# Kernel optimization log

Hardware: AMD Instinct MI355X
Metric: run time of the kernel (lower is better)

Reference implementation:

```python
import jax, jax.numpy as jnp
import numpy as np

N = 100000   # nodes
E = 640000   # edges
IN = 256     # raw input feature dim
D = 128      # post-MLP node feature dim (fixed in FilterGNN)


def setup_inputs() -> dict:
    key = jax.random.key(0)
    ks = jax.random.split(key, 10)
    x = jax.random.normal(ks[0], (N, IN), jnp.float32)
    alpha = jax.random.uniform(ks[1], (E, 1), jnp.float32)  # edge gate logits in [0,1)
    edge_index = jax.random.randint(ks[2], (2, E), 0, N, dtype=jnp.int32)
    norm = jnp.ones((E,), jnp.float32)  # passed to message in the original but unused
    # MLP `lin`: in_channels -> 512 -> 256 -> 128 (kaiming-normal weights, zero bias)
    def kaiming(k, fan_out, fan_in):
        return jax.random.normal(k, (fan_out, fan_in), jnp.float32) * jnp.sqrt(2.0 / fan_in)
    W1 = kaiming(ks[3], 512, IN); b1 = jnp.zeros((512,), jnp.float32)
    W2 = kaiming(ks[4], 256, 512); b2 = jnp.zeros((256,), jnp.float32)
    W3 = kaiming(ks[5], D, 256);  b3 = jnp.zeros((D,), jnp.float32)
    return {"x": x, "alpha": alpha, "edge_index": edge_index, "norm": norm,
            "W1": W1, "b1": b1, "W2": W2, "b2": b2, "W3": W3, "b3": b3}


def reference(x, alpha, edge_index, norm, W1, b1, W2, b2, W3, b3):
    # FilterGNN.lin: Linear-Tanh-Linear-Tanh-Linear  -> [N, 128]
    h = jnp.tanh(x @ W1.T + b1)
    h = jnp.tanh(h @ W2.T + b2)
    h = h @ W3.T + b3
    # FilterGraphConv1: gather x_j, elementwise relu gate, scatter-mean over targets.
    # (The [-1, H, C] view with H*C = 128 is a pure reshape; the gate broadcasts
    #  over all features, so the math is identical without the head split.)
    src, dst = edge_index[0], edge_index[1]
    gate = 2.0 * jax.nn.relu(jax.lax.stop_gradient(alpha) - 0.5)  # [E, 1]
    msg = h[src] * gate                                           # [E, 128] gather + gate
    sums = jax.ops.segment_sum(msg, dst, num_segments=N)          # [N, 128]
    cnt = jax.ops.segment_sum(jnp.ones((E,), h.dtype), dst, num_segments=N)
    out = sums / jnp.maximum(cnt, 1.0)[:, None]                   # scatter-mean (0 if no edges)
    return out
```

## Files before the change

### kernel.cpp

```cpp
#include <hip/hip_runtime.h>

typedef __attribute__((ext_vector_type(8))) short short8;
typedef __attribute__((ext_vector_type(4))) float f32x4;

__device__ __forceinline__ unsigned short f2bf(float f) {
    union { float f; unsigned u; } v; v.f = f;
    unsigned r = v.u + 0x7FFFu + ((v.u >> 16) & 1u);
    return (unsigned short)(r >> 16);
}
__device__ __forceinline__ float bf2f(unsigned short h) {
    union { unsigned u; float f; } v; v.u = ((unsigned)h) << 16;
    return v.f;
}

__device__ __forceinline__ float tanh_fast(float x) {
    float xc = fminf(fmaxf(x, -9.0f), 9.0f);
    float t  = __expf(2.0f * xc);
    return (t - 1.0f) * __builtin_amdgcn_rcpf(t + 1.0f);
}

__device__ __forceinline__ unsigned long long pack4(float4 v) {
    return (unsigned long long)f2bf(v.x)
         | ((unsigned long long)f2bf(v.y) << 16)
         | ((unsigned long long)f2bf(v.z) << 32)
         | ((unsigned long long)f2bf(v.w) << 48);
}

#define GLD16(gptr, lptr)                                                     \
    __builtin_amdgcn_global_load_lds(                                         \
        (const __attribute__((address_space(1))) unsigned int*)(gptr),        \
        (__attribute__((address_space(3))) unsigned int*)(lptr), 16, 0, 0)

__global__ __launch_bounds__(256) void cast_w(
    const float* __restrict__ W1, unsigned short* __restrict__ w1bf,
    const float* __restrict__ W2, unsigned short* __restrict__ w2bf,
    const float* __restrict__ W3, unsigned short* __restrict__ w3bf)
{
    int t = blockIdx.x * 256 + threadIdx.x;
    const float* s; unsigned short* d; int q;
    if (t < 32768)      { s = W1; d = w1bf; q = t; }
    else if (t < 65536) { s = W2; d = w2bf; q = t - 32768; }
    else if (t < 73728) { s = W3; d = w3bf; q = t - 65536; }
    else return;
    int base = q * 4;
    float4 v = *(const float4*)(s + base);
    *(unsigned long long*)(d + base) = pack4(v);
}

__global__ __launch_bounds__(256) void gemm1(
    const float* __restrict__ x, const unsigned short* __restrict__ W1,
    const float* __restrict__ b1, unsigned short* __restrict__ C, int M)
{
    __shared__ __align__(16) short xs[128 * 256];
    __shared__ __align__(16) short Bs[128 * 64];

    const int tid  = threadIdx.x;
    const int wave = tid >> 6;
    const int lane = tid & 63;
    const int m0 = blockIdx.x * 128;
    const int wm = (wave >> 1) * 64;
    const int wn = (wave & 1) * 64;
    const int lm = lane & 15;
    const int quad = lane >> 4;
    const int srow = lane >> 3;
    const int scol = ((lane & 7) ^ srow) * 8;

    #pragma unroll 4
    for (int j = 0; j < 16; ++j) {
        int idx = j * 256 + tid;
        int r = idx >> 5, c = idx & 31;
        int gr = m0 + r; if (gr >= M) gr = M - 1;
        const float* p = x + (size_t)gr * 256 + c * 8;
        float4 a0 = *(const float4*)(p);
        float4 a1 = *(const float4*)(p + 4);
        unsigned long long* d = (unsigned long long*)
            &xs[r * 256 + (c >> 3) * 64 + (((c & 7) ^ (r & 7)) * 8)];
        d[0] = pack4(a0); d[1] = pack4(a1);
    }

    for (int nh = 0; nh < 4; ++nh) {
        const int n0 = nh * 128;
        f32x4 acc[4][4] = {};
        for (int kt = 0; kt < 4; ++kt) {
            const int k0 = kt * 64;
            #pragma unroll
            for (int i = 0; i < 4; ++i) {
                int r0 = wave * 32 + i * 8;
                GLD16(W1 + (size_t)(n0 + r0 + srow) * 256 + k0 + scol, &Bs[r0 * 64]);
            }
            __syncthreads();
            #pragma unroll
            for (int ks = 0; ks < 2; ++ks) {
                short8 af[4], bf_[4];
                const int cc = (((ks * 4 + quad) ^ (lm & 7)) * 8);
                #pragma unroll
                for (int i = 0; i < 4; ++i) {
                    af[i]  = *(const short8*)&xs[(wm + i * 16 + lm) * 256 + k0 + cc];
                    bf_[i] = *(const short8*)&Bs[(wn + i * 16 + lm) * 64 + cc];
                }
                #pragma unroll
                for (int im = 0; im < 4; ++im)
                    #pragma unroll
                    for (int in = 0; in < 4; ++in)
                        acc[im][in] = __builtin_amdgcn_mfma_f32_16x16x32_bf16(
                            af[im], bf_[in], acc[im][in], 0, 0, 0);
            }
            __syncthreads();
        }
        #pragma unroll
        for (int in = 0; in < 4; ++in) {
            int gn = n0 + wn + in * 16 + lm;
            float bb = b1[gn];
            #pragma unroll
            for (int im = 0; im < 4; ++im) {
                #pragma unroll
                for (int r = 0; r < 4; ++r) {
                    int gm = m0 + wm + im * 16 + quad * 4 + r;
                    if (gm < M)
                        C[(size_t)gm * 512 + gn] = f2bf(tanh_fast(acc[im][in][r] + bb));
                }
            }
        }
    }
}

__global__ __launch_bounds__(256) void gemm23(
    const unsigned short* __restrict__ h1, const unsigned short* __restrict__ W2,
    const float* __restrict__ b2, const unsigned short* __restrict__ W3,
    const float* __restrict__ b3, unsigned short* __restrict__ hout, int M)
{
    __shared__ __align__(16) short As[64][64];
    __shared__ __align__(16) short Bs[256][64];
    __shared__ __align__(16) short h2s[64][264];

    const int tid  = threadIdx.x;
    const int wave = tid >> 6;
    const int lane = tid & 63;
    const int m0 = blockIdx.x * 64;
    const int wm = (wave >> 1) * 32;
    const int lm = lane & 15;
    const int quad = lane >> 4;
    const int srow = lane >> 3;
    const int scol = ((lane & 7) ^ srow) * 8;
    const int cc0 = (quad ^ (lm & 7)) * 8;
    const int cc1 = ((4 + quad) ^ (lm & 7)) * 8;

    {
        const int wn = (wave & 1) * 128;
        f32x4 acc[2][8] = {};
        for (int k0 = 0; k0 < 512; k0 += 64) {
            #pragma unroll
            for (int i = 0; i < 2; ++i) {
                int r0 = wave * 16 + i * 8;
                int gr = m0 + r0 + srow; if (gr >= M) gr = M - 1;
                GLD16(h1 + (size_t)gr * 512 + k0 + scol, &As[r0][0]);
            }
            #pragma unroll
            for (int i = 0; i < 8; ++i) {
                int r0 = wave * 64 + i * 8;
                GLD16(W2 + (size_t)(r0 + srow) * 512 + k0 + scol, &Bs[r0][0]);
            }
            __syncthreads();
            #pragma unroll
            for (int ks = 0; ks < 64; ks += 32) {
                const int cc = (ks == 0) ? cc0 : cc1;
                short8 af[2], bf_[8];
                #pragma unroll
                for (int i = 0; i < 2; ++i) af[i]  = *(const short8*)&As[wm + i * 16 + lm][cc];
                #pragma unroll
                for (int i = 0; i < 8; ++i) bf_[i] = *(const short8*)&Bs[wn + i * 16 + lm][cc];
                #pragma unroll
                for (int im = 0; im < 2; ++im)
                    #pragma unroll
                    for (int in = 0; in < 8; ++in)
                        acc[im][in] = __builtin_amdgcn_mfma_f32_16x16x32_bf16(
                            af[im], bf_[in], acc[im][in], 0, 0, 0);
            }
            __syncthreads();
        }
        #pragma unroll
        for (int im = 0; im < 2; ++im) {
            int rb = wm + im * 16 + quad * 4;
            #pragma unroll
            for (int in = 0; in < 8; ++in) {
                int col = wn + in * 16 + lm;
                float bv = b2[col];
                #pragma unroll
                for (int r = 0; r < 4; ++r)
                    h2s[rb + r][col] = (short)f2bf(tanh_fast(acc[im][in][r] + bv));
            }
        }
    }
    __syncthreads();

    {
        const int wn = (wave & 1) * 64;
        short (*Bs3)[64] = (short(*)[64])&Bs[0][0];
        f32x4 acc[2][4] = {};
        for (int k0 = 0; k0 < 256; k0 += 64) {
            #pragma unroll
            for (int i = 0; i < 4; ++i) {
                int r0 = wave * 32 + i * 8;
                GLD16(W3 + (size_t)(r0 + srow) * 256 + k0 + scol, &Bs3[r0][0]);
            }
            __syncthreads();
            #pragma unroll
            for (int ks = 0; ks < 64; ks += 32) {
                const int cc = (ks == 0) ? cc0 : cc1;
                short8 af[2], bf_[4];
                #pragma unroll
                for (int i = 0; i < 2; ++i)
                    af[i] = *(const short8*)&h2s[wm + i * 16 + lm][k0 + ks + quad * 8];
                #pragma unroll
                for (int i = 0; i < 4; ++i)
                    bf_[i] = *(const short8*)&Bs3[wn + i * 16 + lm][cc];
                #pragma unroll
                for (int im = 0; im < 2; ++im)
                    #pragma unroll
                    for (int in = 0; in < 4; ++in)
                        acc[im][in] = __builtin_amdgcn_mfma_f32_16x16x32_bf16(
                            af[im], bf_[in], acc[im][in], 0, 0, 0);
            }
            __syncthreads();
        }
        #pragma unroll
        for (int im = 0; im < 2; ++im) {
            int gm_base = m0 + wm + im * 16 + quad * 4;
            #pragma unroll
            for (int in = 0; in < 4; ++in) {
                int gn = wn + in * 16 + lm;
                float bv = b3[gn];
                #pragma unroll
                for (int r = 0; r < 4; ++r) {
                    int gm = gm_base + r;
                    if (gm < M)
                        hout[(size_t)gm * 128 + gn] = f2bf(acc[im][in][r] + bv);
                }
            }
        }
    }
}

__global__ __launch_bounds__(256) void edge_hist(
    const int* __restrict__ ei, const float* __restrict__ alpha,
    unsigned long long* __restrict__ deg, int E)
{
    int e = blockIdx.x * 256 + threadIdx.x;
    if (e >= E) return;
    int dst = ei[E + e];
    float gate = 2.0f * fmaxf(alpha[e] - 0.5f, 0.0f);
    atomicAdd(&deg[dst], 0x100000000ULL | (gate > 0.0f ? 1ULL : 0ULL));
}

__global__ __launch_bounds__(256) void scan1(
    const unsigned long long* __restrict__ deg, int* __restrict__ rowptr,
    int* __restrict__ cursor, int* __restrict__ partials, int N)
{
    __shared__ int sums[256];
    int base = blockIdx.x * 1024 + threadIdx.x * 4;
    int v[4];
    #pragma unroll
    for (int i = 0; i < 4; ++i) {
        int idx = base + i;
        v[i] = (idx < N) ? (int)(deg[idx] & 0xffffffffULL) : 0;
    }
    int s = v[0] + v[1] + v[2] + v[3];
    sums[threadIdx.x] = s;
    __syncthreads();
    for (int off = 1; off < 256; off <<= 1) {
        int t = (threadIdx.x >= off) ? sums[threadIdx.x - off] : 0;
        __syncthreads();
        sums[threadIdx.x] += t;
        __syncthreads();
    }
    int excl = sums[threadIdx.x] - s;
    if (threadIdx.x == 255) partials[blockIdx.x] = sums[255];
    int run = excl;
    #pragma unroll
    for (int i = 0; i < 4; ++i) {
        int idx = base + i;
        if (idx < N) { rowptr[idx] = run; cursor[idx] = run; }
        run += v[i];
    }
}

__global__ __launch_bounds__(256) void scan2(int* __restrict__ partials, int nb)
{
    __shared__ int s[256];
    int v = (threadIdx.x < nb) ? partials[threadIdx.x] : 0;
    s[threadIdx.x] = v;
    __syncthreads();
    for (int off = 1; off < 256; off <<= 1) {
        int t = (threadIdx.x >= off) ? s[threadIdx.x - off] : 0;
        __syncthreads();
        s[threadIdx.x] += t;
        __syncthreads();
    }
    partials[threadIdx.x] = s[threadIdx.x] - v;
}

__global__ __launch_bounds__(256) void edge_fill(
    const int* __restrict__ ei, const float* __restrict__ alpha,
    int* __restrict__ cursor, const int* __restrict__ partials,
    int2* __restrict__ recs, int E)
{
    int e = blockIdx.x * 256 + threadIdx.x;
    if (e >= E) return;
    float gate = 2.0f * fmaxf(alpha[e] - 0.5f, 0.0f);
    if (gate > 0.0f) {
        int dst = ei[E + e];
        int src = ei[e];
        int pos = atomicAdd(&cursor[dst], 1) + partials[dst >> 10];
        recs[pos] = make_int2(src, __float_as_int(gate));
    }
}

__global__ __launch_bounds__(256) void node_gather(
    const unsigned short* __restrict__ h, const unsigned long long* __restrict__ deg,
    const int* __restrict__ rowptr, const int* __restrict__ partials,
    const int2* __restrict__ recs, float* __restrict__ out, int N)
{
    int wave = threadIdx.x >> 6;
    int lane = threadIdx.x & 63;
    int node = blockIdx.x * 4 + wave;
    if (node >= N) return;
    unsigned long long d = deg[node];
    int dAll  = __builtin_amdgcn_readfirstlane((int)(d >> 32));
    int dG    = __builtin_amdgcn_readfirstlane((int)(d & 0xffffffffULL));
    int start = __builtin_amdgcn_readfirstlane(rowptr[node] + partials[node >> 10]);
    int qw = lane >> 4, ql = lane & 15;
    float a[8] = {};
    for (int j = 0; j < dG; j += 4) {
        int jj = j + qw;
        int idx = start + (jj < dG ? jj : dG - 1);
        int2 rec = recs[idx];
        float gate = (jj < dG) ? __int_as_float(rec.y) : 0.0f;
        uint4 u = *(const uint4*)(h + ((size_t)rec.x << 7) + ql * 8);
        a[0] += bf2f((unsigned short)(u.x & 0xffffu)) * gate;
        a[1] += bf2f((unsigned short)(u.x >> 16)) * gate;
        a[2] += bf2f((unsigned short)(u.y & 0xffffu)) * gate;
        a[3] += bf2f((unsigned short)(u.y >> 16)) * gate;
        a[4] += bf2f((unsigned short)(u.z & 0xffffu)) * gate;
        a[5] += bf2f((unsigned short)(u.z >> 16)) * gate;
        a[6] += bf2f((unsigned short)(u.w & 0xffffu)) * gate;
        a[7] += bf2f((unsigned short)(u.w >> 16)) * gate;
    }
    #pragma unroll
    for (int i = 0; i < 8; ++i) {
        a[i] += __shfl_xor(a[i], 16);
        a[i] += __shfl_xor(a[i], 32);
    }
    if (qw == 0) {
        float inv = 1.0f / fmaxf((float)dAll, 1.0f);
        float* op = out + ((size_t)node << 7) + ql * 8;
        *(float4*)(op)     = make_float4(a[0] * inv, a[1] * inv, a[2] * inv, a[3] * inv);
        *(float4*)(op + 4) = make_float4(a[4] * inv, a[5] * inv, a[6] * inv, a[7] * inv);
    }
}

extern "C" void kernel_launch(void* const* d_in, const int* in_sizes, int n_in,
                              void* d_out, int out_size, void* d_ws, size_t ws_size,
                              hipStream_t stream) {
    const float* x     = (const float*)d_in[0];
    const float* alpha = (const float*)d_in[1];
    const int*   ei    = (const int*)d_in[2];
    const float* W1 = (const float*)d_in[4];
    const float* b1 = (const float*)d_in[5];
    const float* W2 = (const float*)d_in[6];
    const float* b2 = (const float*)d_in[7];
    const float* W3 = (const float*)d_in[8];
    const float* b3 = (const float*)d_in[9];
    float* out = (float*)d_out;

    const int N = in_sizes[0] / 256;
    const int E = in_sizes[1];
    const int H1 = 512, D = 128;

    char* ws = (char*)d_ws;
    size_t off = 0;
    auto take = [&](size_t bytes) { char* p = ws + off; off = (off + bytes + 255) & ~(size_t)255; return p; };
    unsigned short* h1bf = (unsigned short*)take((size_t)N * H1 * 2);
    unsigned short* hbf  = (unsigned short*)take((size_t)N * D  * 2);
    unsigned short* w1bf = (unsigned short*)take((size_t)H1 * 256 * 2);
    unsigned short* w2bf = (unsigned short*)take((size_t)256 * H1 * 2);
    unsigned short* w3bf = (unsigned short*)take((size_t)D * 256 * 2);

    char* cbase = (char*)h1bf;
    size_t coff = 0;
    auto ctake = [&](size_t bytes) { char* p = cbase + coff; coff = (coff + bytes + 255) & ~(size_t)255; return p; };
    unsigned long long* deg = (unsigned long long*)ctake((size_t)N * 8);
    int*  rowptr   = (int*)ctake((size_t)N * 4);
    int*  cursor   = (int*)ctake((size_t)N * 4);
    int*  partials = (int*)ctake(256 * 4);
    int2* recs     = (int2*)ctake((size_t)E * 8);

    dim3 blk(256);

    cast_w<<<288, blk, 0, stream>>>(W1, w1bf, W2, w2bf, W3, w3bf);
    const int mblk = (N + 127) / 128;
    gemm1<<<dim3(mblk), blk, 0, stream>>>(x, w1bf, b1, h1bf, N);
    gemm23<<<(N + 63) / 64, blk, 0, stream>>>(h1bf, w2bf, b2, w3bf, b3, hbf, N);

    hipMemsetAsync(deg, 0, (size_t)N * 8, stream);
    edge_hist<<<(E + 255) / 256, blk, 0, stream>>>(ei, alpha, deg, E);
    const int nb1 = (N + 1023) / 1024;
    scan1<<<nb1, blk, 0, stream>>>(deg, rowptr, cursor, partials, N);
    scan2<<<1, blk, 0, stream>>>(partials, nb1);
    edge_fill<<<(E + 255) / 256, blk, 0, stream>>>(ei, alpha, cursor, partials, recs, E);

    node_gather<<<(N + 3) / 4, blk, 0, stream>>>(hbf, deg, rowptr, partials, recs, out, N);
}
```

Measured before the change: 446.4 us.

## Restructure gemm1 to 64-row tiles with 8 waves reading W1 directly

Rewrites the first MLP GEMM so each 512-thread block handles 64 rows. Each of the 8 waves owns a 64-column slice of the 512 outputs, and B fragments are read straight from the bf16 W1 in global memory instead of being staged through LDS. This removes the per-k-tile LDS staging, the barriers around it and the outer loop over output halves, and halves the x tile in LDS so more blocks can be resident. In exchange every wave fetches W1 from global or L2 with no reuse through shared memory, and occupancy is pinned by launch bounds of 512 threads and 2 blocks.

```diff
diff --git a/kernel.cpp b/kernel.cpp
--- a/kernel.cpp
+++ b/kernel.cpp
@@ -47,27 +47,22 @@
     *(unsigned long long*)(d + base) = pack4(v);
 }
 
-__global__ __launch_bounds__(256) void gemm1(
+__global__ __launch_bounds__(512, 2) void gemm1(
     const float* __restrict__ x, const unsigned short* __restrict__ W1,
     const float* __restrict__ b1, unsigned short* __restrict__ C, int M)
 {
-    __shared__ __align__(16) short xs[128 * 256];
-    __shared__ __align__(16) short Bs[128 * 64];
+    __shared__ __align__(16) short xs[64 * 256];
 
     const int tid  = threadIdx.x;
     const int wave = tid >> 6;
     const int lane = tid & 63;
-    const int m0 = blockIdx.x * 128;
-    const int wm = (wave >> 1) * 64;
-    const int wn = (wave & 1) * 64;
-    const int lm = lane & 15;
+    const int m0   = blockIdx.x * 64;
+    const int lm   = lane & 15;
     const int quad = lane >> 4;
-    const int srow = lane >> 3;
-    const int scol = ((lane & 7) ^ srow) * 8;
-
-    #pragma unroll 4
-    for (int j = 0; j < 16; ++j) {
-        int idx = j * 256 + tid;
+
+    #pragma unroll
+    for (int j = 0; j < 4; ++j) {
+        int idx = j * 512 + tid;
         int r = idx >> 5, c = idx & 31;
         int gr = m0 + r; if (gr >= M) gr = M - 1;
         const float* p = x + (size_t)gr * 256 + c * 8;
@@ -77,48 +72,40 @@
             &xs[r * 256 + (c >> 3) * 64 + (((c & 7) ^ (r & 7)) * 8)];
         d[0] = pack4(a0); d[1] = pack4(a1);
     }
-
-    for (int nh = 0; nh < 4; ++nh) {
-        const int n0 = nh * 128;
-        f32x4 acc[4][4] = {};
-        for (int kt = 0; kt < 4; ++kt) {
-            const int k0 = kt * 64;
-            #pragma unroll
-            for (int i = 0; i < 4; ++i) {
-                int r0 = wave * 32 + i * 8;
-                GLD16(W1 + (size_t)(n0 + r0 + srow) * 256 + k0 + scol, &Bs[r0 * 64]);
-            }
-            __syncthreads();
-            #pragma unroll
-            for (int ks = 0; ks < 2; ++ks) {
-                short8 af[4], bf_[4];
-                const int cc = (((ks * 4 + quad) ^ (lm & 7)) * 8);
-                #pragma unroll
-                for (int i = 0; i < 4; ++i) {
-                    af[i]  = *(const short8*)&xs[(wm + i * 16 + lm) * 256 + k0 + cc];
-                    bf_[i] = *(const short8*)&Bs[(wn + i * 16 + lm) * 64 + cc];
-                }
-                #pragma unroll
-                for (int im = 0; im < 4; ++im)
-                    #pragma unroll
-                    for (int in = 0; in < 4; ++in)
-                        acc[im][in] = __builtin_amdgcn_mfma_f32_16x16x32_bf16(
-                            af[im], bf_[in], acc[im][in], 0, 0, 0);
-            }
-            __syncthreads();
-        }
-        #pragma unroll
-        for (int in = 0; in < 4; ++in) {
-            int gn = n0 + wn + in * 16 + lm;
-            float bb = b1[gn];
-            #pragma unroll
-            for (int im = 0; im < 4; ++im) {
-                #pragma unroll
-                for (int r = 0; r < 4; ++r) {
-                    int gm = m0 + wm + im * 16 + quad * 4 + r;
-                    if (gm < M)
-                        C[(size_t)gm * 512 + gn] = f2bf(tanh_fast(acc[im][in][r] + bb));
-                }
+    __syncthreads();
+
+    const int n0 = wave * 64;
+    f32x4 acc[4][4] = {};
+    #pragma unroll
+    for (int ks = 0; ks < 8; ++ks) {
+        const int k = ks * 32 + quad * 8;
+        const int c = k >> 3;
+        short8 af[4], bv[4];
+        #pragma unroll
+        for (int i = 0; i < 4; ++i) {
+            int r = i * 16 + lm;
+            af[i] = *(const short8*)&xs[r * 256 + (c >> 3) * 64 + (((c & 7) ^ (r & 7)) * 8)];
+            bv[i] = *(const short8*)&W1[(size_t)(n0 + i * 16 + lm) * 256 + k];
+        }
+        #pragma unroll
+        for (int im = 0; im < 4; ++im)
+            #pragma unroll
+            for (int in = 0; in < 4; ++in)
+                acc[im][in] = __builtin_amdgcn_mfma_f32_16x16x32_bf16(
+                    af[im], bv[in], acc[im][in], 0, 0, 0);
+    }
+
+    #pragma unroll
+    for (int in = 0; in < 4; ++in) {
+        int gn = n0 + in * 16 + lm;
+        float bb = b1[gn];
+        #pragma unroll
+        for (int im = 0; im < 4; ++im) {
+            #pragma unroll
+            for (int r = 0; r < 4; ++r) {
+                int gm = m0 + im * 16 + quad * 4 + r;
+                if (gm < M)
+                    C[(size_t)gm * 512 + gn] = f2bf(tanh_fast(acc[im][in][r] + bb));
             }
         }
     }
@@ -397,8 +384,7 @@
     dim3 blk(256);
 
     cast_w<<<288, blk, 0, stream>>>(W1, w1bf, W2, w2bf, W3, w3bf);
-    const int mblk = (N + 127) / 128;
-    gemm1<<<dim3(mblk), blk, 0, stream>>>(x, w1bf, b1, h1bf, N);
+    gemm1<<<(N + 63) / 64, dim3(512), 0, stream>>>(x, w1bf, b1, h1bf, N);
     gemm23<<<(N + 63) / 64, blk, 0, stream>>>(h1bf, w2bf, b2, w3bf, b3, hbf, N);
 
     hipMemsetAsync(deg, 0, (size_t)N * 8, stream);
```

Result: no change. 449.4 us (+0.7%).
